# Kernel tuning notes

Hardware: AMD Instinct MI355X
Metric: run time of the kernel (lower is better)

Reference implementation:

```python
import jax, jax.numpy as jnp
import numpy as np

N_NODES = 20000
N_EDGES = 400000
IN_DIM = 512
OUT_DIM = 1
HIDDEN = [512, 512, 512, 256, OUT_DIM]


def _glorot(key, fan_in, fan_out):
    lim = np.sqrt(6.0 / (fan_in + fan_out)).astype(np.float32)
    return jax.random.uniform(key, (fan_in, fan_out), jnp.float32, -lim, lim)


def setup_inputs() -> dict:
    key = jax.random.key(0)
    ks = jax.random.split(key, 16)
    x = jax.random.normal(ks[0], (N_NODES, IN_DIM), jnp.float32)
    edge_index = jax.random.randint(ks[1], (2, N_EDGES), 0, N_NODES, jnp.int64)
    edge_attr = jax.random.uniform(ks[2], (N_EDGES,), jnp.float32)
    inp = {"x": x, "edge_index": edge_index, "edge_attr": edge_attr}
    dims = [IN_DIM] + HIDDEN
    for i in range(5):
        inp[f"W{i+1}"] = _glorot(ks[3 + i], dims[i], dims[i + 1])
        inp[f"b{i+1}"] = jnp.zeros((dims[i + 1],), jnp.float32)
    return inp


def gcn_layer(x, W, b, src, dst, ew, n):
    # x: [N, Fin] -> [N, Fout]; GCNConv: D^{-1/2}(A+I)D^{-1/2} X W + b
    h = x @ W
    loop = jnp.arange(n)
    src_f = jnp.concatenate([src, loop])
    dst_f = jnp.concatenate([dst, loop])
    ew_f = jnp.concatenate([ew, jnp.ones((n,), x.dtype)])  # self-loop weight 1
    deg = jax.ops.segment_sum(ew_f, dst_f, num_segments=n)
    dinv = jnp.where(deg > 0, jax.lax.rsqrt(deg), 0.0)
    norm = dinv[src_f] * ew_f * dinv[dst_f]  # [E+N]
    out = jax.ops.segment_sum(norm[:, None] * h[src_f], dst_f, num_segments=n)
    return out + b


def reference(x, edge_index, edge_attr, W1, b1, W2, b2, W3, b3, W4, b4, W5, b5):
    src, dst = edge_index[0], edge_index[1]
    n = x.shape[0]
    h = jax.nn.relu(gcn_layer(x, W1, b1, src, dst, edge_attr, n))
    h = jax.nn.relu(gcn_layer(h, W2, b2, src, dst, edge_attr, n))
    h = jax.nn.relu(gcn_layer(h, W3, b3, src, dst, edge_attr, n))
    h = jax.nn.relu(gcn_layer(h, W4, b4, src, dst, edge_attr, n))
    h = gcn_layer(h, W5, b5, src, dst, edge_attr, n)
    return h
```

## Files before the change

### kernel.cpp

```cpp
#include <hip/hip_runtime.h>
#include <cstdint>
#include <cstddef>

#define N_NODES 20000
#define N_EDGES 400000
#define NBLK 79
#define MPAD 20128

typedef __attribute__((ext_vector_type(8))) short bf16x8;
typedef __attribute__((ext_vector_type(4))) float f32x4;
typedef __attribute__((ext_vector_type(2))) int i32x2;

__device__ __forceinline__ float bf2f(unsigned short u) {
    return __uint_as_float(((unsigned int)u) << 16);
}
__device__ __forceinline__ unsigned short f2bf(float f) {
    unsigned int x = __float_as_uint(f);
    unsigned int lsb = (x >> 16) & 1u;
    x += 0x7fffu + lsb;
    return (unsigned short)(x >> 16);
}

__device__ __forceinline__ float ldF(const void* p, size_t i, bool bf) {
    return bf ? bf2f(((const unsigned short*)p)[i]) : ((const float*)p)[i];
}

__device__ __forceinline__ void gl2lds16(const unsigned short* g, unsigned short* l) {
    __builtin_amdgcn_global_load_lds(
        (const __attribute__((address_space(1))) void*)g,
        (__attribute__((address_space(3))) void*)l, 16, 0, 0);
}

__global__ void k_detect(const unsigned int* __restrict__ xw, const int* __restrict__ raw,
                         int* __restrict__ flag) {
    int lane = threadIdx.x;
    int cnt = 0, nz = 0;
    for (int i = lane; i < 256; i += 64) {
        unsigned short lo = (unsigned short)(xw[i] & 0xffffu);
        int e = (lo >> 7) & 0xff;
        if (e >= 110 && e <= 135) cnt++;
    }
    for (int i = 2 * lane + 1; i < 512; i += 128)
        if (raw[i] != 0) nz++;
#pragma unroll
    for (int off = 32; off > 0; off >>= 1) {
        cnt += __shfl_down(cnt, off);
        nz  += __shfl_down(nz, off);
    }
    if (lane == 0) {
        flag[0] = (cnt >= 128) ? 1 : 0;
        flag[1] = (nz == 0) ? 1 : 0;
    }
}

__global__ void k_canon_deg(const int* __restrict__ raw, const void* __restrict__ ew,
                            const int* __restrict__ flagp,
                            float* __restrict__ deg, int* __restrict__ counts) {
    bool bf = (flagp[0] != 0);
    int is64 = flagp[1];
    int e = blockIdx.x * blockDim.x + threadIdx.x;
    if (e >= N_EDGES) return;
    int d;
    if (is64) d = raw[2 * (N_EDGES + e)];
    else      d = raw[N_EDGES + e];
    atomicAdd(&deg[d], ldF(ew, e, bf));
    atomicAdd(&counts[d], 1);
}

__global__ __launch_bounds__(256) void k_part(const int* __restrict__ counts,
                                              const float* __restrict__ deg,
                                              float* __restrict__ dinv,
                                              float* __restrict__ selfnorm,
                                              int* __restrict__ bsum) {
    __shared__ int s[256];
    int t = threadIdx.x;
    int i = blockIdx.x * 256 + t;
    int c = (i < N_NODES) ? counts[i] : 0;
    if (i < N_NODES) {
        float d = deg[i] + 1.0f;
        float r = rsqrtf(d);
        dinv[i] = r;
        selfnorm[i] = r * r;
    }
    s[t] = c;
    __syncthreads();
    for (int off = 128; off > 0; off >>= 1) {
        if (t < off) s[t] += s[t + off];
        __syncthreads();
    }
    if (t == 0) bsum[blockIdx.x] = s[0];
}

__global__ void k_scanb(const int* __restrict__ bsum, int* __restrict__ bofs,
                        int* __restrict__ rowptr) {
    __shared__ int s[128];
    int t = threadIdx.x;
    int v = (t < NBLK) ? bsum[t] : 0;
    s[t] = v;
    __syncthreads();
    for (int off = 1; off < 128; off <<= 1) {
        int u = (t >= off) ? s[t - off] : 0;
        __syncthreads();
        s[t] += u;
        __syncthreads();
    }
    if (t < NBLK) bofs[t] = s[t] - v;
    if (t == NBLK - 1) rowptr[N_NODES] = s[t];
}

__global__ __launch_bounds__(256) void k_row(const int* __restrict__ counts,
                                             const int* __restrict__ bofs,
                                             int* __restrict__ rowptr) {
    __shared__ int s[256];
    int t = threadIdx.x;
    int b = blockIdx.x;
    int i = b * 256 + t;
    int c = (i < N_NODES) ? counts[i] : 0;
    s[t] = c;
    __syncthreads();
    for (int off = 1; off < 256; off <<= 1) {
        int u = (t >= off) ? s[t - off] : 0;
        __syncthreads();
        s[t] += u;
        __syncthreads();
    }
    if (i < N_NODES) rowptr[i] = bofs[b] + s[t] - c;
}

__global__ void k_csr(const int* __restrict__ raw, const void* __restrict__ ew,
                      const int* __restrict__ flagp,
                      const float* __restrict__ dinv, const int* __restrict__ rowptr,
                      int* __restrict__ fill, int* __restrict__ csr_pair) {
    bool bf = (flagp[0] != 0);
    int is64 = flagp[1];
    int e = blockIdx.x * blockDim.x + threadIdx.x;
    if (e >= N_EDGES) return;
    int s, d;
    if (is64) { s = raw[2 * e]; d = raw[2 * (N_EDGES + e)]; }
    else      { s = raw[e];     d = raw[N_EDGES + e]; }
    int p = rowptr[d] + atomicAdd(&fill[d], 1);
    float nrm = dinv[s] * ldF(ew, e, bf) * dinv[d];
    i32x2 pv;
    pv.x = s;
    pv.y = __float_as_int(nrm);
    *(i32x2*)(csr_pair + 2 * (size_t)p) = pv;
}

__global__ __launch_bounds__(256) void k_prep(const void* __restrict__ x,
                                              const void* __restrict__ W1,
                                              const void* __restrict__ W2,
                                              const void* __restrict__ W3,
                                              const void* __restrict__ W4,
                                              const void* __restrict__ b1,
                                              const void* __restrict__ b2,
                                              const void* __restrict__ b3,
                                              const void* __restrict__ b4,
                                              const void* __restrict__ W5,
                                              const int* __restrict__ flagp,
                                              unsigned short* __restrict__ P,
                                              unsigned short* __restrict__ Wp,
                                              float* __restrict__ biasf) {
    bool bf = (*flagp != 0);
    int b = blockIdx.x;
    int t = threadIdx.x;
    if (b < 10000) {
        if (bf) return;
        int i = b * 256 + t;
        float4 v = ((const float4*)x)[i];
        unsigned int lo = (unsigned int)f2bf(v.x) | ((unsigned int)f2bf(v.y) << 16);
        unsigned int hi = (unsigned int)f2bf(v.z) | ((unsigned int)f2bf(v.w) << 16);
        ((uint2*)P)[i] = make_uint2(lo, hi);
    } else if (b < 10448) {
        int gidx = (b - 10000) * 256 + t;
        if (gidx >= 114688) return;
        const void* W;
        int idx = gidx, N, nbl;
        if (gidx < 32768)      { W = W1; N = 512; nbl = 5; }
        else if (gidx < 65536) { W = W2; N = 512; nbl = 5; idx -= 32768; }
        else if (gidx < 98304) { W = W3; N = 512; nbl = 5; idx -= 65536; }
        else                   { W = W4; N = 256; nbl = 4; idx -= 98304; }
        int lane = idx & 63;
        int blk = idx >> 6;
        int nb = blk & ((1 << nbl) - 1);
        int kb = blk >> nbl;
        int n = (nb << 4) + (lane & 15);
        int kbase = (kb << 5) + ((lane >> 4) << 3);
        unsigned short o[8];
#pragma unroll
        for (int j = 0; j < 8; ++j)
            o[j] = f2bf(ldF(W, (size_t)(kbase + j) * N + n, bf));
        *(uint4*)(&Wp[(size_t)gidx * 8]) = *(const uint4*)o;
    } else {
        int i = (b - 10448) * 256 + t;
        if (i >= 2304) return;
        if (i < 2048) {
            int L = i >> 9, r = i & 511;
            if (L == 3 && r >= 256) return;
            const void* bb = (L == 0) ? b1 : (L == 1) ? b2 : (L == 2) ? b3 : b4;
            biasf[i] = ldF(bb, r, bf);
        } else {
            biasf[i] = ldF(W5, i - 2048, bf);
        }
    }
}

__global__ __launch_bounds__(256) void k_gemm_mfma(const unsigned short* __restrict__ Abase,
                                                   const unsigned short* __restrict__ Aalt,
                                                   const int* __restrict__ flagp,
                                                   const unsigned short* __restrict__ Bp,
                                                   unsigned short* __restrict__ C,
                                                   int M, int K, int N) {
    const int AP = 72;
    __shared__ __align__(16) unsigned short As[128 * AP];
    __shared__ __align__(16) unsigned short Bs[2 * 8 * 512];
    const unsigned short* A = (*flagp != 0) ? Aalt : Abase;
    int tid = threadIdx.x;
    int lane = tid & 63;
    int wave = tid >> 6;
    int wr = wave >> 1, wc = wave & 1;
    int row0 = blockIdx.x * 128;
    int col0 = blockIdx.y * 128;
    int nbt = N >> 4;
    int q = lane >> 4;
    int mm = lane & 15;

    f32x4 acc[4][4] = {};

    for (int kb2 = 0; kb2 < (K >> 6); ++kb2) {
        const unsigned short* breg0 = Bp + (((size_t)(2 * kb2) * nbt + (col0 >> 4)) << 9);
        const unsigned short* breg1 = Bp + (((size_t)(2 * kb2 + 1) * nbt + (col0 >> 4)) << 9);
        gl2lds16(breg0 + (size_t)tid * 8, &Bs[(size_t)tid * 8]);
        gl2lds16(breg0 + (size_t)(tid + 256) * 8, &Bs[(size_t)(tid + 256) * 8]);
        gl2lds16(breg1 + (size_t)tid * 8, &Bs[4096 + (size_t)tid * 8]);
        gl2lds16(breg1 + (size_t)(tid + 256) * 8, &Bs[4096 + (size_t)(tid + 256) * 8]);
#pragma unroll
        for (int i = 0; i < 4; ++i) {
            int c = tid + i * 256;
            int row = c >> 3, kq = c & 7;
            int grow = min(row0 + row, M - 1);
            uint4 v = *(const uint4*)(&A[(size_t)grow * K + (kb2 << 6) + (kq << 3)]);
            *(uint4*)(&As[row * AP + (kq << 3)]) = v;
        }
        __syncthreads();
#pragma unroll
        for (int kk = 0; kk < 2; ++kk) {
            bf16x8 af[4], bfr[4];
#pragma unroll
            for (int mb = 0; mb < 4; ++mb)
                af[mb] = *(const bf16x8*)(&As[(wr * 64 + mb * 16 + mm) * AP + kk * 32 + q * 8]);
#pragma unroll
            for (int nb = 0; nb < 4; ++nb)
                bfr[nb] = *(const bf16x8*)(&Bs[kk * 4096 + ((wc * 4 + nb) * 64 + lane) * 8]);
#pragma unroll
            for (int mb = 0; mb < 4; ++mb)
#pragma unroll
                for (int nb = 0; nb < 4; ++nb)
                    acc[mb][nb] = __builtin_amdgcn_mfma_f32_16x16x32_bf16(
                        af[mb], bfr[nb], acc[mb][nb], 0, 0, 0);
        }
        __syncthreads();
    }
#pragma unroll
    for (int mb = 0; mb < 4; ++mb) {
#pragma unroll
        for (int r = 0; r < 4; ++r) {
            int grow = row0 + wr * 64 + mb * 16 + q * 4 + r;
            if (grow < M) {
#pragma unroll
                for (int nb = 0; nb < 4; ++nb) {
                    int gcol = col0 + wc * 64 + nb * 16 + mm;
                    C[(size_t)grow * N + gcol] = f2bf(acc[mb][nb][r]);
                }
            }
        }
    }
}

template <int W>
__device__ __forceinline__ void ldrow(const unsigned short* h, size_t row, int F, int lane,
                                      unsigned int* u) {
    const unsigned int* p = (const unsigned int*)(h + row * F) + lane * W;
    if constexpr (W == 4) {
        uint4 v = *(const uint4*)p; u[0] = v.x; u[1] = v.y; u[2] = v.z; u[3] = v.w;
    } else {
        uint2 v = *(const uint2*)p; u[0] = v.x; u[1] = v.y;
    }
}
template <int W>
__device__ __forceinline__ void fmarow(const unsigned int* u, float w, float* acc) {
#pragma unroll
    for (int k = 0; k < W; ++k) {
        acc[2 * k]     = fmaf(bf2f((unsigned short)(u[k] & 0xffffu)), w, acc[2 * k]);
        acc[2 * k + 1] = fmaf(bf2f((unsigned short)(u[k] >> 16)),     w, acc[2 * k + 1]);
    }
}

__global__ __launch_bounds__(64) void k_agg_w(const unsigned short* __restrict__ h,
                                              const int* __restrict__ rowptr,
                                              const int* __restrict__ csr_pair,
                                              const float* __restrict__ selfnorm,
                                              const float* __restrict__ biasf,
                                              unsigned short* __restrict__ out) {
    constexpr int F = 512;
    int lane = threadIdx.x;
    int chunk = blockIdx.x & 3;
    int node = blockIdx.x >> 2;
    int e0 = rowptr[node], e1 = rowptr[node + 1];
    float sn = selfnorm[node];
    const unsigned short* hb = h + chunk * 128 + lane * 2;

    float a0, a1;
    {
        unsigned int u = *(const unsigned int*)(hb + (size_t)node * F);
        a0 = sn * bf2f((unsigned short)(u & 0xffffu));
        a1 = sn * bf2f((unsigned short)(u >> 16));
    }
    const i32x2* pairs = (const i32x2*)csr_pair;
    int j = e0;
    for (; j + 7 < e1; j += 8) {
        i32x2 p0 = pairs[j],     p1 = pairs[j + 1], p2 = pairs[j + 2], p3 = pairs[j + 3];
        i32x2 p4 = pairs[j + 4], p5 = pairs[j + 5], p6 = pairs[j + 6], p7 = pairs[j + 7];
        unsigned int u0 = *(const unsigned int*)(hb + (size_t)p0.x * F);
        unsigned int u1 = *(const unsigned int*)(hb + (size_t)p1.x * F);
        unsigned int u2 = *(const unsigned int*)(hb + (size_t)p2.x * F);
        unsigned int u3 = *(const unsigned int*)(hb + (size_t)p3.x * F);
        unsigned int u4 = *(const unsigned int*)(hb + (size_t)p4.x * F);
        unsigned int u5 = *(const unsigned int*)(hb + (size_t)p5.x * F);
        unsigned int u6 = *(const unsigned int*)(hb + (size_t)p6.x * F);
        unsigned int u7 = *(const unsigned int*)(hb + (size_t)p7.x * F);
        float w0 = __int_as_float(p0.y), w1 = __int_as_float(p1.y);
        float w2 = __int_as_float(p2.y), w3 = __int_as_float(p3.y);
        float w4 = __int_as_float(p4.y), w5 = __int_as_float(p5.y);
        float w6 = __int_as_float(p6.y), w7 = __int_as_float(p7.y);
        a0 = fmaf(bf2f((unsigned short)(u0 & 0xffffu)), w0, a0);
        a1 = fmaf(bf2f((unsigned short)(u0 >> 16)),     w0, a1);
        a0 = fmaf(bf2f((unsigned short)(u1 & 0xffffu)), w1, a0);
        a1 = fmaf(bf2f((unsigned short)(u1 >> 16)),     w1, a1);
        a0 = fmaf(bf2f((unsigned short)(u2 & 0xffffu)), w2, a0);
        a1 = fmaf(bf2f((unsigned short)(u2 >> 16)),     w2, a1);
        a0 = fmaf(bf2f((unsigned short)(u3 & 0xffffu)), w3, a0);
        a1 = fmaf(bf2f((unsigned short)(u3 >> 16)),     w3, a1);
        a0 = fmaf(bf2f((unsigned short)(u4 & 0xffffu)), w4, a0);
        a1 = fmaf(bf2f((unsigned short)(u4 >> 16)),     w4, a1);
        a0 = fmaf(bf2f((unsigned short)(u5 & 0xffffu)), w5, a0);
        a1 = fmaf(bf2f((unsigned short)(u5 >> 16)),     w5, a1);
        a0 = fmaf(bf2f((unsigned short)(u6 & 0xffffu)), w6, a0);
        a1 = fmaf(bf2f((unsigned short)(u6 >> 16)),     w6, a1);
        a0 = fmaf(bf2f((unsigned short)(u7 & 0xffffu)), w7, a0);
        a1 = fmaf(bf2f((unsigned short)(u7 >> 16)),     w7, a1);
    }
    for (; j + 3 < e1; j += 4) {
        i32x2 p0 = pairs[j], p1 = pairs[j + 1], p2 = pairs[j + 2], p3 = pairs[j + 3];
        unsigned int u0 = *(const unsigned int*)(hb + (size_t)p0.x * F);
        unsigned int u1 = *(const unsigned int*)(hb + (size_t)p1.x * F);
        unsigned int u2 = *(const unsigned int*)(hb + (size_t)p2.x * F);
        unsigned int u3 = *(const unsigned int*)(hb + (size_t)p3.x * F);
        float w0 = __int_as_float(p0.y), w1 = __int_as_float(p1.y);
        float w2 = __int_as_float(p2.y), w3 = __int_as_float(p3.y);
        a0 = fmaf(bf2f((unsigned short)(u0 & 0xffffu)), w0, a0);
        a1 = fmaf(bf2f((unsigned short)(u0 >> 16)),     w0, a1);
        a0 = fmaf(bf2f((unsigned short)(u1 & 0xffffu)), w1, a0);
        a1 = fmaf(bf2f((unsigned short)(u1 >> 16)),     w1, a1);
        a0 = fmaf(bf2f((unsigned short)(u2 & 0xffffu)), w2, a0);
        a1 = fmaf(bf2f((unsigned short)(u2 >> 16)),     w2, a1);
        a0 = fmaf(bf2f((unsigned short)(u3 & 0xffffu)), w3, a0);
        a1 = fmaf(bf2f((unsigned short)(u3 >> 16)),     w3, a1);
    }
    for (; j < e1; ++j) {
        i32x2 p0 = pairs[j];
        unsigned int u0 = *(const unsigned int*)(hb + (size_t)p0.x * F);
        float w0 = __int_as_float(p0.y);
        a0 = fmaf(bf2f((unsigned short)(u0 & 0xffffu)), w0, a0);
        a1 = fmaf(bf2f((unsigned short)(u0 >> 16)),     w0, a1);
    }
    {
        const float* bp = biasf + chunk * 128 + lane * 2;
        a0 = fmaxf(a0 + bp[0], 0.f);
        a1 = fmaxf(a1 + bp[1], 0.f);
        unsigned int o = (unsigned int)f2bf(a0) | ((unsigned int)f2bf(a1) << 16);
        *(unsigned int*)(out + (size_t)node * F + chunk * 128 + lane * 2) = o;
    }
}

__global__ __launch_bounds__(64) void k_agg_fuse(const unsigned short* __restrict__ h,
                                                 const int* __restrict__ rowptr,
                                                 const int* __restrict__ csr_pair,
                                                 const float* __restrict__ selfnorm,
                                                 const float* __restrict__ biasf,
                                                 const float* __restrict__ w5f,
                                                 float* __restrict__ h5) {
    constexpr int F = 256, FPL = 4, W = 2;
    int lane = threadIdx.x;
    int node = blockIdx.x;
    int e0 = rowptr[node], e1 = rowptr[node + 1];
    float sn = selfnorm[node];

    float acc[FPL];
    {
        unsigned int u[W];
        ldrow<W>(h, (size_t)node, F, lane, u);
#pragma unroll
        for (int k = 0; k < W; ++k) {
            acc[2 * k]     = sn * bf2f((unsigned short)(u[k] & 0xffffu));
            acc[2 * k + 1] = sn * bf2f((unsigned short)(u[k] >> 16));
        }
    }
    const i32x2* pairs = (const i32x2*)csr_pair;
    int j = e0;
    for (; j + 7 < e1; j += 8) {
        i32x2 p0 = pairs[j],     p1 = pairs[j + 1], p2 = pairs[j + 2], p3 = pairs[j + 3];
        i32x2 p4 = pairs[j + 4], p5 = pairs[j + 5], p6 = pairs[j + 6], p7 = pairs[j + 7];
        unsigned int u0[W], u1[W], u2[W], u3[W], u4[W], u5[W], u6[W], u7[W];
        ldrow<W>(h, (size_t)p0.x, F, lane, u0);
        ldrow<W>(h, (size_t)p1.x, F, lane, u1);
        ldrow<W>(h, (size_t)p2.x, F, lane, u2);
        ldrow<W>(h, (size_t)p3.x, F, lane, u3);
        ldrow<W>(h, (size_t)p4.x, F, lane, u4);
        ldrow<W>(h, (size_t)p5.x, F, lane, u5);
        ldrow<W>(h, (size_t)p6.x, F, lane, u6);
        ldrow<W>(h, (size_t)p7.x, F, lane, u7);
        fmarow<W>(u0, __int_as_float(p0.y), acc);
        fmarow<W>(u1, __int_as_float(p1.y), acc);
        fmarow<W>(u2, __int_as_float(p2.y), acc);
        fmarow<W>(u3, __int_as_float(p3.y), acc);
        fmarow<W>(u4, __int_as_float(p4.y), acc);
        fmarow<W>(u5, __int_as_float(p5.y), acc);
        fmarow<W>(u6, __int_as_float(p6.y), acc);
        fmarow<W>(u7, __int_as_float(p7.y), acc);
    }
    for (; j + 3 < e1; j += 4) {
        i32x2 p0 = pairs[j], p1 = pairs[j + 1], p2 = pairs[j + 2], p3 = pairs[j + 3];
        unsigned int u0[W], u1[W], u2[W], u3[W];
        ldrow<W>(h, (size_t)p0.x, F, lane, u0);
        ldrow<W>(h, (size_t)p1.x, F, lane, u1);
        ldrow<W>(h, (size_t)p2.x, F, lane, u2);
        ldrow<W>(h, (size_t)p3.x, F, lane, u3);
        fmarow<W>(u0, __int_as_float(p0.y), acc);
        fmarow<W>(u1, __int_as_float(p1.y), acc);
        fmarow<W>(u2, __int_as_float(p2.y), acc);
        fmarow<W>(u3, __int_as_float(p3.y), acc);
    }
    for (; j < e1; ++j) {
        i32x2 p0 = pairs[j];
        unsigned int u0[W];
        ldrow<W>(h, (size_t)p0.x, F, lane, u0);
        fmarow<W>(u0, __int_as_float(p0.y), acc);
    }
    const float* bp = biasf + lane * FPL;
    const float* wp = w5f + lane * FPL;
    float partial = 0.f;
#pragma unroll
    for (int k = 0; k < FPL; ++k)
        partial += fmaxf(acc[k] + bp[k], 0.f) * wp[k];
#pragma unroll
    for (int off = 32; off > 0; off >>= 1)
        partial += __shfl_xor(partial, off);
    if (lane == 0) h5[node] = partial;
}

__global__ void k_final(const float* __restrict__ h5, const int* __restrict__ rowptr,
                        const int* __restrict__ csr_pair,
                        const float* __restrict__ selfnorm,
                        const void* __restrict__ b5, const int* __restrict__ flagp,
                        void* __restrict__ out) {
    bool bf = (*flagp != 0);
    int i = blockIdx.x * blockDim.x + threadIdx.x;
    if (i >= N_NODES) return;
    float acc = selfnorm[i] * h5[i];
    int e0 = rowptr[i], e1 = rowptr[i + 1];
    for (int j = e0; j < e1; ++j) {
        int s = csr_pair[2 * (size_t)j];
        float w = __int_as_float(csr_pair[2 * (size_t)j + 1]);
        acc += w * h5[s];
    }
    acc += ldF(b5, 0, bf);
    if (bf) ((unsigned short*)out)[i] = f2bf(acc);
    else    ((float*)out)[i] = acc;
}

extern "C" void kernel_launch(void* const* d_in, const int* in_sizes, int n_in,
                              void* d_out, int out_size, void* d_ws, size_t ws_size,
                              hipStream_t stream) {
    const void* x  = d_in[0];
    const int*  ei = (const int*)d_in[1];
    const void* ea = d_in[2];
    const void* W1 = d_in[3];
    const void* b1 = d_in[4];
    const void* W2 = d_in[5];
    const void* b2 = d_in[6];
    const void* W3 = d_in[7];
    const void* b3 = d_in[8];
    const void* W4 = d_in[9];
    const void* b4 = d_in[10];
    const void* W5 = d_in[11];
    const void* b5 = d_in[12];

    char* ws = (char*)d_ws;
    size_t off = 0;
    auto take = [&](size_t bytes) -> void* {
        off = (off + 255) & ~(size_t)255;
        void* p = ws + off;
        off += bytes;
        return p;
    };
    int*   flagp    = (int*)take(2 * sizeof(int));
    float* deg      = (float*)take(N_NODES * sizeof(float));
    int*   counts   = (int*)take(N_NODES * sizeof(int));
    int*   fill     = (int*)take(N_NODES * sizeof(int));
    size_t zspan    = (size_t)((char*)(fill + N_NODES) - (char*)deg);
    float* dinv     = (float*)take(N_NODES * sizeof(float));
    float* selfnorm = (float*)take(N_NODES * sizeof(float));
    float* h5       = (float*)take(N_NODES * sizeof(float));
    float* biasf    = (float*)take(2304 * sizeof(float));
    int*   bsum     = (int*)take(128 * sizeof(int));
    int*   bofs     = (int*)take(128 * sizeof(int));
    int*   rowptr   = (int*)take((N_NODES + 1) * sizeof(int));
    int*   csr_pair = (int*)take((size_t)N_EDGES * 2 * sizeof(int));
    unsigned short* Wp = (unsigned short*)take((size_t)114688 * 8 * sizeof(unsigned short));
    unsigned short* P  = (unsigned short*)take((size_t)MPAD * 512 * sizeof(unsigned short));
    unsigned short* H  = (unsigned short*)take((size_t)MPAD * 512 * sizeof(unsigned short));

    (void)hipMemsetAsync(deg, 0, zspan, stream);

    const int EB = (N_EDGES + 255) / 256;
    const int NB = (N_NODES + 255) / 256;

    k_detect<<<1, 64, 0, stream>>>((const unsigned int*)x, ei, flagp);
    k_canon_deg<<<EB, 256, 0, stream>>>(ei, ea, flagp, deg, counts);
    k_part<<<NB, 256, 0, stream>>>(counts, deg, dinv, selfnorm, bsum);
    k_scanb<<<1, 128, 0, stream>>>(bsum, bofs, rowptr);
    k_row<<<NB, 256, 0, stream>>>(counts, bofs, rowptr);
    k_csr<<<EB, 256, 0, stream>>>(ei, ea, flagp, dinv, rowptr, fill, csr_pair);

    k_prep<<<10457, 256, 0, stream>>>(x, W1, W2, W3, W4, b1, b2, b3, b4, W5, flagp,
                                      P, Wp, biasf);

    const int MB128 = (N_NODES + 127) / 128;

    k_gemm_mfma<<<dim3(MB128, 4), 256, 0, stream>>>(P, (const unsigned short*)x, flagp,
                                                    Wp, H, N_NODES, 512, 512);
    k_agg_w<<<N_NODES * 4, 64, 0, stream>>>(H, rowptr, csr_pair, selfnorm, biasf, P);
    k_gemm_mfma<<<dim3(MB128, 4), 256, 0, stream>>>(P, P, flagp,
                                                    Wp + (size_t)32768 * 8, H,
                                                    N_NODES, 512, 512);
    k_agg_w<<<N_NODES * 4, 64, 0, stream>>>(H, rowptr, csr_pair, selfnorm, biasf + 512, P);
    k_gemm_mfma<<<dim3(MB128, 4), 256, 0, stream>>>(P, P, flagp,
                                                    Wp + (size_t)65536 * 8, H,
                                                    N_NODES, 512, 512);
    k_agg_w<<<N_NODES * 4, 64, 0, stream>>>(H, rowptr, csr_pair, selfnorm, biasf + 1024, P);
    k_gemm_mfma<<<dim3(MB128, 2), 256, 0, stream>>>(P, P, flagp,
                                                    Wp + (size_t)98304 * 8, H,
                                                    N_NODES, 512, 256);
    k_agg_fuse<<<N_NODES, 64, 0, stream>>>(H, rowptr, csr_pair, selfnorm,
                                           biasf + 1536, biasf + 2048, h5);

    k_final<<<NB, 256, 0, stream>>>(h5, rowptr, csr_pair, selfnorm, b5, flagp,
                                    d_out);
}
```

Baseline: 410.8 us.

## Fuse x fp32-to-bf16 conversion into first GEMM and split fused aggregation

The separate pass that converted x to bf16 inside k_prep is removed. The first GEMM now reads fp32 x directly and converts to bf16 while staging A tiles into LDS, which avoids writing and re-reading a 20 MB bf16 copy. The layer-4 fused aggregation now runs two 64-lane blocks per node, each covering 128 features, and combines their partial dot products into h5 with atomicAdd; h5 is moved into the memset-zeroed span to support this. The cost is extra VALU work and wider fp32 loads inside the GEMM, and atomics in the aggregation.

```diff
diff --git a/kernel.cpp b/kernel.cpp
--- a/kernel.cpp
+++ b/kernel.cpp
@@ -146,8 +146,7 @@
     *(i32x2*)(csr_pair + 2 * (size_t)p) = pv;
 }
 
-__global__ __launch_bounds__(256) void k_prep(const void* __restrict__ x,
-                                              const void* __restrict__ W1,
+__global__ __launch_bounds__(256) void k_prep(const void* __restrict__ W1,
                                               const void* __restrict__ W2,
                                               const void* __restrict__ W3,
                                               const void* __restrict__ W4,
@@ -157,22 +156,13 @@
                                               const void* __restrict__ b4,
                                               const void* __restrict__ W5,
                                               const int* __restrict__ flagp,
-                                              unsigned short* __restrict__ P,
                                               unsigned short* __restrict__ Wp,
                                               float* __restrict__ biasf) {
     bool bf = (*flagp != 0);
     int b = blockIdx.x;
     int t = threadIdx.x;
-    if (b < 10000) {
-        if (bf) return;
-        int i = b * 256 + t;
-        float4 v = ((const float4*)x)[i];
-        unsigned int lo = (unsigned int)f2bf(v.x) | ((unsigned int)f2bf(v.y) << 16);
-        unsigned int hi = (unsigned int)f2bf(v.z) | ((unsigned int)f2bf(v.w) << 16);
-        ((uint2*)P)[i] = make_uint2(lo, hi);
-    } else if (b < 10448) {
-        int gidx = (b - 10000) * 256 + t;
-        if (gidx >= 114688) return;
+    if (b < 448) {
+        int gidx = b * 256 + t;
         const void* W;
         int idx = gidx, N, nbl;
         if (gidx < 32768)      { W = W1; N = 512; nbl = 5; }
@@ -191,7 +181,7 @@
             o[j] = f2bf(ldF(W, (size_t)(kbase + j) * N + n, bf));
         *(uint4*)(&Wp[(size_t)gidx * 8]) = *(const uint4*)o;
     } else {
-        int i = (b - 10448) * 256 + t;
+        int i = (b - 448) * 256 + t;
         if (i >= 2304) return;
         if (i < 2048) {
             int L = i >> 9, r = i & 511;
@@ -205,15 +195,19 @@
 }
 
 __global__ __launch_bounds__(256) void k_gemm_mfma(const unsigned short* __restrict__ Abase,
-                                                   const unsigned short* __restrict__ Aalt,
+                                                   const void* __restrict__ Xraw,
                                                    const int* __restrict__ flagp,
+                                                   int useX,
                                                    const unsigned short* __restrict__ Bp,
                                                    unsigned short* __restrict__ C,
                                                    int M, int K, int N) {
     const int AP = 72;
     __shared__ __align__(16) unsigned short As[128 * AP];
     __shared__ __align__(16) unsigned short Bs[2 * 8 * 512];
-    const unsigned short* A = (*flagp != 0) ? Aalt : Abase;
+    bool bf = (*flagp != 0);
+    bool cvt = useX && !bf;
+    const unsigned short* A = useX ? (const unsigned short*)Xraw : Abase;
+    const float* Af = (const float*)Xraw;
     int tid = threadIdx.x;
     int lane = tid & 63;
     int wave = tid >> 6;
@@ -238,8 +232,20 @@
             int c = tid + i * 256;
             int row = c >> 3, kq = c & 7;
             int grow = min(row0 + row, M - 1);
-            uint4 v = *(const uint4*)(&A[(size_t)grow * K + (kb2 << 6) + (kq << 3)]);
-            *(uint4*)(&As[row * AP + (kq << 3)]) = v;
+            size_t idx = (size_t)grow * K + (kb2 << 6) + (kq << 3);
+            if (!cvt) {
+                uint4 v = *(const uint4*)(&A[idx]);
+                *(uint4*)(&As[row * AP + (kq << 3)]) = v;
+            } else {
+                float4 v0 = *(const float4*)(Af + idx);
+                float4 v1 = *(const float4*)(Af + idx + 4);
+                uint4 o;
+                o.x = (unsigned int)f2bf(v0.x) | ((unsigned int)f2bf(v0.y) << 16);
+                o.y = (unsigned int)f2bf(v0.z) | ((unsigned int)f2bf(v0.w) << 16);
+                o.z = (unsigned int)f2bf(v1.x) | ((unsigned int)f2bf(v1.y) << 16);
+                o.w = (unsigned int)f2bf(v1.z) | ((unsigned int)f2bf(v1.w) << 16);
+                *(uint4*)(&As[row * AP + (kq << 3)]) = o;
+            }
         }
         __syncthreads();
 #pragma unroll
@@ -273,25 +279,6 @@
                 }
             }
         }
-    }
-}
-
-template <int W>
-__device__ __forceinline__ void ldrow(const unsigned short* h, size_t row, int F, int lane,
-                                      unsigned int* u) {
-    const unsigned int* p = (const unsigned int*)(h + row * F) + lane * W;
-    if constexpr (W == 4) {
-        uint4 v = *(const uint4*)p; u[0] = v.x; u[1] = v.y; u[2] = v.z; u[3] = v.w;
-    } else {
-        uint2 v = *(const uint2*)p; u[0] = v.x; u[1] = v.y;
-    }
-}
-template <int W>
-__device__ __forceinline__ void fmarow(const unsigned int* u, float w, float* acc) {
-#pragma unroll
-    for (int k = 0; k < W; ++k) {
-        acc[2 * k]     = fmaf(bf2f((unsigned short)(u[k] & 0xffffu)), w, acc[2 * k]);
-        acc[2 * k + 1] = fmaf(bf2f((unsigned short)(u[k] >> 16)),     w, acc[2 * k + 1]);
     }
 }
 
@@ -389,73 +376,71 @@
                                                  const float* __restrict__ biasf,
                                                  const float* __restrict__ w5f,
                                                  float* __restrict__ h5) {
-    constexpr int F = 256, FPL = 4, W = 2;
+    constexpr int F = 256;
     int lane = threadIdx.x;
-    int node = blockIdx.x;
+    int chunk = blockIdx.x & 1;
+    int node = blockIdx.x >> 1;
     int e0 = rowptr[node], e1 = rowptr[node + 1];
     float sn = selfnorm[node];
-
-    float acc[FPL];
+    const unsigned short* hb = h + chunk * 128 + lane * 2;
+
+    float a0, a1;
     {
-        unsigned int u[W];
-        ldrow<W>(h, (size_t)node, F, lane, u);
-#pragma unroll
-        for (int k = 0; k < W; ++k) {
-            acc[2 * k]     = sn * bf2f((unsigned short)(u[k] & 0xffffu));
-            acc[2 * k + 1] = sn * bf2f((unsigned short)(u[k] >> 16));
-        }
+        unsigned int u = *(const unsigned int*)(hb + (size_t)node * F);
+        a0 = sn * bf2f((unsigned short)(u & 0xffffu));
+        a1 = sn * bf2f((unsigned short)(u >> 16));
     }
     const i32x2* pairs = (const i32x2*)csr_pair;
     int j = e0;
     for (; j + 7 < e1; j += 8) {
         i32x2 p0 = pairs[j],     p1 = pairs[j + 1], p2 = pairs[j + 2], p3 = pairs[j + 3];
         i32x2 p4 = pairs[j + 4], p5 = pairs[j + 5], p6 = pairs[j + 6], p7 = pairs[j + 7];
-        unsigned int u0[W], u1[W], u2[W], u3[W], u4[W], u5[W], u6[W], u7[W];
-        ldrow<W>(h, (size_t)p0.x, F, lane, u0);
-        ldrow<W>(h, (size_t)p1.x, F, lane, u1);
-        ldrow<W>(h, (size_t)p2.x, F, lane, u2);
-        ldrow<W>(h, (size_t)p3.x, F, lane, u3);
-        ldrow<W>(h, (size_t)p4.x, F, lane, u4);
-        ldrow<W>(h, (size_t)p5.x, F, lane, u5);
-        ldrow<W>(h, (size_t)p6.x, F, lane, u6);
-        ldrow<W>(h, (size_t)p7.x, F, lane, u7);
-        fmarow<W>(u0, __int_as_float(p0.y), acc);
-        fmarow<W>(u1, __int_as_float(p1.y), acc);
-        fmarow<W>(u2, __int_as_float(p2.y), acc);
-        fmarow<W>(u3, __int_as_float(p3.y), acc);
-        fmarow<W>(u4, __int_as_float(p4.y), acc);
-        fmarow<W>(u5, __int_as_float(p5.y), acc);
-        fmarow<W>(u6, __int_as_float(p6.y), acc);
-        fmarow<W>(u7, __int_as_float(p7.y), acc);
-    }
-    for (; j + 3 < e1; j += 4) {
-        i32x2 p0 = pairs[j], p1 = pairs[j + 1], p2 = pairs[j + 2], p3 = pairs[j + 3];
-        unsigned int u0[W], u1[W], u2[W], u3[W];
-        ldrow<W>(h, (size_t)p0.x, F, lane, u0);
-        ldrow<W>(h, (size_t)p1.x, F, lane, u1);
-        ldrow<W>(h, (size_t)p2.x, F, lane, u2);
-        ldrow<W>(h, (size_t)p3.x, F, lane, u3);
-        fmarow<W>(u0, __int_as_float(p0.y), acc);
-        fmarow<W>(u1, __int_as_float(p1.y), acc);
-        fmarow<W>(u2, __int_as_float(p2.y), acc);
-        fmarow<W>(u3, __int_as_float(p3.y), acc);
+        unsigned int u0 = *(const unsigned int*)(hb + (size_t)p0.x * F);
+        unsigned int u1 = *(const unsigned int*)(hb + (size_t)p1.x * F);
+        unsigned int u2 = *(const unsigned int*)(hb + (size_t)p2.x * F);
+        unsigned int u3 = *(const unsigned int*)(hb + (size_t)p3.x * F);
+        unsigned int u4 = *(const unsigned int*)(hb + (size_t)p4.x * F);
+        unsigned int u5 = *(const unsigned int*)(hb + (size_t)p5.x * F);
+        unsigned int u6 = *(const unsigned int*)(hb + (size_t)p6.x * F);
+        unsigned int u7 = *(const unsigned int*)(hb + (size_t)p7.x * F);
+        float w0 = __int_as_float(p0.y), w1 = __int_as_float(p1.y);
+        float w2 = __int_as_float(p2.y), w3 = __int_as_float(p3.y);
+        float w4 = __int_as_float(p4.y), w5 = __int_as_float(p5.y);
+        float w6 = __int_as_float(p6.y), w7 = __int_as_float(p7.y);
+        a0 = fmaf(bf2f((unsigned short)(u0 & 0xffffu)), w0, a0);
+        a1 = fmaf(bf2f((unsigned short)(u0 >> 16)),     w0, a1);
+        a0 = fmaf(bf2f((unsigned short)(u1 & 0xffffu)), w1, a0);
+        a1 = fmaf(bf2f((unsigned short)(u1 >> 16)),     w1, a1);
+        a0 = fmaf(bf2f((unsigned short)(u2 & 0xffffu)), w2, a0);
+        a1 = fmaf(bf2f((unsigned short)(u2 >> 16)),     w2, a1);
+        a0 = fmaf(bf2f((unsigned short)(u3 & 0xffffu)), w3, a0);
+        a1 = fmaf(bf2f((unsigned short)(u3 >> 16)),     w3, a1);
+        a0 = fmaf(bf2f((unsigned short)(u4 & 0xffffu)), w4, a0);
+        a1 = fmaf(bf2f((unsigned short)(u4 >> 16)),     w4, a1);
+        a0 = fmaf(bf2f((unsigned short)(u5 & 0xffffu)), w5, a0);
+        a1 = fmaf(bf2f((unsigned short)(u5 >> 16)),     w5, a1);
+        a0 = fmaf(bf2f((unsigned short)(u6 & 0xffffu)), w6, a0);
+        a1 = fmaf(bf2f((unsigned short)(u6 >> 16)),     w6, a1);
+        a0 = fmaf(bf2f((unsigned short)(u7 & 0xffffu)), w7, a0);
+        a1 = fmaf(bf2f((unsigned short)(u7 >> 16)),     w7, a1);
     }
     for (; j < e1; ++j) {
         i32x2 p0 = pairs[j];
-        unsigned int u0[W];
-        ldrow<W>(h, (size_t)p0.x, F, lane, u0);
-        fmarow<W>(u0, __int_as_float(p0.y), acc);
-    }
-    const float* bp = biasf + lane * FPL;
-    const float* wp = w5f + lane * FPL;
-    float partial = 0.f;
-#pragma unroll
-    for (int k = 0; k < FPL; ++k)
-        partial += fmaxf(acc[k] + bp[k], 0.f) * wp[k];
-#pragma unroll
-    for (int off = 32; off > 0; off >>= 1)
-        partial += __shfl_xor(partial, off);
-    if (lane == 0) h5[node] = partial;
+        unsigned int u0 = *(const unsigned int*)(hb + (size_t)p0.x * F);
+        float w0 = __int_as_float(p0.y);
+        a0 = fmaf(bf2f((unsigned short)(u0 & 0xffffu)), w0, a0);
+        a1 = fmaf(bf2f((unsigned short)(u0 >> 16)),     w0, a1);
+    }
+    {
+        const float* bp = biasf + chunk * 128 + lane * 2;
+        const float* wp = w5f + chunk * 128 + lane * 2;
+        float partial = fmaxf(a0 + bp[0], 0.f) * wp[0]
+                      + fmaxf(a1 + bp[1], 0.f) * wp[1];
+#pragma unroll
+        for (int off = 32; off > 0; off >>= 1)
+            partial += __shfl_xor(partial, off);
+        if (lane == 0) atomicAdd(h5 + node, partial);
+    }
 }
 
 __global__ void k_final(const float* __restrict__ h5, const int* __restrict__ rowptr,
@@ -507,10 +492,10 @@
     float* deg      = (float*)take(N_NODES * sizeof(float));
     int*   counts   = (int*)take(N_NODES * sizeof(int));
     int*   fill     = (int*)take(N_NODES * sizeof(int));
-    size_t zspan    = (size_t)((char*)(fill + N_NODES) - (char*)deg);
+    float* h5       = (float*)take(N_NODES * sizeof(float));
+    size_t zspan    = (size_t)((char*)(h5 + N_NODES) - (char*)deg);
     float* dinv     = (float*)take(N_NODES * sizeof(float));
     float* selfnorm = (float*)take(N_NODES * sizeof(float));
-    float* h5       = (float*)take(N_NODES * sizeof(float));
     float* biasf    = (float*)take(2304 * sizeof(float));
     int*   bsum     = (int*)take(128 * sizeof(int));
     int*   bofs     = (int*)take(128 * sizeof(int));
@@ -524,6 +509,8 @@
 
     const int EB = (N_EDGES + 255) / 256;
     const int NB = (N_NODES + 255) / 256;
+    const int AGW = N_NODES * 4;
+    const int AGF = N_NODES * 2;
 
     k_detect<<<1, 64, 0, stream>>>((const unsigned int*)x, ei, flagp);
     k_canon_deg<<<EB, 256, 0, stream>>>(ei, ea, flagp, deg, counts);
@@ -532,27 +519,27 @@
     k_row<<<NB, 256, 0, stream>>>(counts, bofs, rowptr);
     k_csr<<<EB, 256, 0, stream>>>(ei, ea, flagp, dinv, rowptr, fill, csr_pair);
 
-    k_prep<<<10457, 256, 0, stream>>>(x, W1, W2, W3, W4, b1, b2, b3, b4, W5, flagp,
-                                      P, Wp, biasf);
+    k_prep<<<457, 256, 0, stream>>>(W1, W2, W3, W4, b1, b2, b3, b4, W5, flagp,
+                                    Wp, biasf);
 
     const int MB128 = (N_NODES + 127) / 128;
 
-    k_gemm_mfma<<<dim3(MB128, 4), 256, 0, stream>>>(P, (const unsigned short*)x, flagp,
+    k_gemm_mfma<<<dim3(MB128, 4), 256, 0, stream>>>(P, x, flagp, 1,
                                                     Wp, H, N_NODES, 512, 512);
-    k_agg_w<<<N_NODES * 4, 64, 0, stream>>>(H, rowptr, csr_pair, selfnorm, biasf, P);
-    k_gemm_mfma<<<dim3(MB128, 4), 256, 0, stream>>>(P, P, flagp,
+    k_agg_w<<<AGW, 64, 0, stream>>>(H, rowptr, csr_pair, selfnorm, biasf, P);
+    k_gemm_mfma<<<dim3(MB128, 4), 256, 0, stream>>>(P, x, flagp, 0,
                                                     Wp + (size_t)32768 * 8, H,
                                                     N_NODES, 512, 512);
-    k_agg_w<<<N_NODES * 4, 64, 0, stream>>>(H, rowptr, csr_pair, selfnorm, biasf + 512, P);
-    k_gemm_mfma<<<dim3(MB128, 4), 256, 0, stream>>>(P, P, flagp,
+    k_agg_w<<<AGW, 64, 0, stream>>>(H, rowptr, csr_pair, selfnorm, biasf + 512, P);
+    k_gemm_mfma<<<dim3(MB128, 4), 256, 0, stream>>>(P, x, flagp, 0,
                                                     Wp + (size_t)65536 * 8, H,
                                                     N_NODES, 512, 512);
-    k_agg_w<<<N_NODES * 4, 64, 0, stream>>>(H, rowptr, csr_pair, selfnorm, biasf + 1024, P);
-    k_gemm_mfma<<<dim3(MB128, 2), 256, 0, stream>>>(P, P, flagp,
+    k_agg_w<<<AGW, 64, 0, stream>>>(H, rowptr, csr_pair, selfnorm, biasf + 1024, P);
+    k_gemm_mfma<<<dim3(MB128, 2), 256, 0, stream>>>(P, x, flagp, 0,
                                                     Wp + (size_t)98304 * 8, H,
                                                     N_NODES, 512, 256);
-    k_agg_fuse<<<N_NODES, 64, 0, stream>>>(H, rowptr, csr_pair, selfnorm,
-                                           biasf + 1536, biasf + 2048, h5);
+    k_agg_fuse<<<AGF, 64, 0, stream>>>(H, rowptr, csr_pair, selfnorm,
+                                       biasf + 1536, biasf + 2048, h5);
 
     k_final<<<NB, 256, 0, stream>>>(h5, rowptr, csr_pair, selfnorm, b5, flagp,
                                     d_out);
```

New measurement: 436.0 us. 6.1% more time.
